# Kernel optimization log

Hardware: AMD Instinct MI355X
Metric: run time of the kernel (lower is better)

The kernel has to match this reference:

```python
import jax, jax.numpy as jnp
import numpy as np

B = 2048        # patients (segments)
K = 4           # images per patient
C = 1280        # backbone_out (tf_efficientnet_b0)
PAIRS = K * (K - 1) // 2  # torch.combinations -> 6
NCLS = 1
N_DROP = 5


def setup_inputs() -> dict:
    key = jax.random.key(0)
    ks = jax.random.split(key, 8)
    x = jax.random.normal(ks[0], (B * K, C), jnp.float32)  # detached backbone features
    ids2 = jnp.repeat(jnp.arange(B, dtype=jnp.int32), PAIRS)  # segment id per pair
    Wc = jax.random.normal(ks[1], (C, C, 2), jnp.float32) * 0.02  # Conv1d(C,C,k=2) weight
    bc = jnp.zeros((C,), jnp.float32)
    W0 = jax.random.normal(ks[2], (NCLS, C), jnp.float32) * 0.02
    b0 = jnp.zeros((NCLS,), jnp.float32)
    W1 = jax.random.normal(ks[3], (1, C), jnp.float32) * 0.02
    b1 = jnp.zeros((1,), jnp.float32)
    W2 = jax.random.normal(ks[4], (1, C), jnp.float32) * 0.02
    b2 = jnp.zeros((1,), jnp.float32)
    return dict(x=x, ids2=ids2, Wc=Wc, bc=bc, W0=W0, b0=b0, W1=W1, b1=b1, W2=W2, b2=b2)


def reference(x, ids2, Wc, bc, W0, b0, W1, b1, W2, b2):
    # --- pair combinations within each patient group of K images ---
    ii, jj = np.triu_indices(K, 1)               # static [PAIRS]
    xg = x.reshape(B, K, C)
    xa = xg[:, ii].reshape(B * PAIRS, C)         # first element of each pair
    xb = xg[:, jj].reshape(B * PAIRS, C)         # second element
    # Conv1d(C, C, kernel=2) over the length-2 pair sequence + ReLU
    xc = jax.nn.relu(xa @ Wc[:, :, 0].T + xb @ Wc[:, :, 1].T + bc)  # [P, C]

    # --- 5 fixed dropout masks (p=0.5, train-mode scaling) ---
    masks = jax.random.bernoulli(jax.random.key(42), 0.5,
                                 (N_DROP, xc.shape[0], C)).astype(xc.dtype) * 2.0
    xd = xc[None] * masks                        # [D, P, C]

    cnt = jax.ops.segment_sum(jnp.ones_like(ids2, dtype=xc.dtype),
                              ids2, num_segments=B)  # [B], == PAIRS

    def agg(W, b):
        # head -> scalar mean over classes -> segment-mean over pairs -> mean over dropouts
        z = (jnp.einsum('dpc,oc->dpo', xd, W) + b).mean(-1)          # [D, P]
        s = jax.vmap(lambda u: jax.ops.segment_sum(u, ids2, num_segments=B))(z)
        return (s / cnt).mean(0)                                      # [B]

    logits = agg(W0, b0)
    logits1 = agg(W1, b1)
    logits2 = agg(W2, b2)
    return jnp.stack([logits, logits1, logits2], axis=1)  # [B, 3]
```

## Files before the change

kernel.cpp:

```cpp
#include <hip/hip_runtime.h>


typedef __attribute__((ext_vector_type(8))) short short8;
typedef __attribute__((ext_vector_type(4))) float f32x4;

#define PLANE 15728640u
#define KS2   (0x1BD11BDAu ^ 42u)

__device__ __forceinline__ unsigned short f2bf(float f) {
  unsigned int u = __builtin_bit_cast(unsigned int, f);
  u = (u + 0x7FFFu + ((u >> 16) & 1u)) >> 16;
  return (unsigned short)u;
}
__device__ __forceinline__ float bf2f(unsigned short h) {
  unsigned int u = ((unsigned int)h) << 16;
  return __builtin_bit_cast(float, u);
}

__global__ __launch_bounds__(256) void prep(
    const float* __restrict__ x, unsigned short* __restrict__ xb,
    const float* __restrict__ Wc, unsigned short* __restrict__ Wb) {
  const int bid = blockIdx.x;
  const int t = threadIdx.x;
  if (bid < 2560) {
#pragma unroll
    for (int p = 0; p < 4; p++) {
      const int i4 = bid * 1024 + p * 256 + t;
      const float4 v = ((const float4*)x)[i4];
      ushort4 o;
      o.x = f2bf(v.x); o.y = f2bf(v.y); o.z = f2bf(v.z); o.w = f2bf(v.w);
      ((ushort4*)xb)[i4] = o;
    }
  } else {
    const int i = (bid - 2560) * 256 + t;
    const int n = i / 640;
    const int cin = (i - n * 640) * 2;
    const float4 v = *(const float4*)(Wc + n * 2560 + cin * 2);
    *(ushort2*)(Wb + n * 2560 + cin) =
        make_ushort2(f2bf(v.x), f2bf(v.z));
    *(ushort2*)(Wb + n * 2560 + 1280 + cin) =
        make_ushort2(f2bf(v.y), f2bf(v.w));
  }
}

__device__ __forceinline__ unsigned int rotl(unsigned int x, int r) {
  return __builtin_amdgcn_alignbit(x, x, 32 - r);
}

__device__ __forceinline__ unsigned int tf_msb5(const unsigned int cbase) {
  unsigned int x0[5], x1[5];
#pragma unroll
  for (int d = 0; d < 5; d++) {
    const unsigned int c = cbase + (unsigned int)d * PLANE;
    x0[d] = c;
    x1[d] = rotl(c, 13) ^ c;
  }
#define R5(r)                                                   \
  _Pragma("unroll") for (int d = 0; d < 5; d++) {               \
    x0[d] += x1[d];                                             \
    x1[d] = rotl(x1[d], (r)) ^ x0[d];                           \
  }
  R5(15) R5(26) R5(6)
#pragma unroll
  for (int d = 0; d < 5; d++) {
    const unsigned int t = x1[d] + (KS2 + 1u);
    x0[d] = x0[d] + t + 42u;
    x1[d] = rotl(t, 17) ^ x0[d];
  }
  R5(29) R5(16) R5(24)
#pragma unroll
  for (int d = 0; d < 5; d++) {
    const unsigned int t = x1[d] + 2u;
    x0[d] = x0[d] + t + KS2;
    x1[d] = rotl(t, 13) ^ x0[d];
  }
  R5(15) R5(26) R5(6)
#pragma unroll
  for (int d = 0; d < 5; d++) {
    const unsigned int t = x1[d] + 45u;
    x0[d] = x0[d] + t;
    x1[d] = rotl(t, 17) ^ x0[d];
  }
  R5(29) R5(16) R5(24)
#pragma unroll
  for (int d = 0; d < 5; d++) {
    const unsigned int t = x1[d] + (KS2 + 4u);
    x0[d] = x0[d] + t + 42u;
    x1[d] = rotl(t, 13) ^ x0[d];
  }
  R5(15) R5(26) R5(6)
#undef R5
  unsigned int z = 0;
#pragma unroll
  for (int d = 0; d < 5; d++)
    z += ((x0[d] + KS2) ^ (x1[d] + 5u)) >> 31;
  return z;
}

#define GL_LDS(g, l) __builtin_amdgcn_global_load_lds( \
    (const __attribute__((address_space(1))) unsigned int*)(g), \
    (__attribute__((address_space(3))) unsigned int*)(l), 16, 0, 0)

__global__ __launch_bounds__(256) void mixed(
    const unsigned short* __restrict__ Xb,
    const unsigned short* __restrict__ Wb,
    unsigned short* __restrict__ U0b,
    unsigned short* __restrict__ U1b)
{
  __shared__ unsigned short sA[128 * 32];
  __shared__ unsigned short sB[128 * 32];
  const int bid = blockIdx.x;
  const int t = threadIdx.x;

  const int id = bid;
  const int xcd = id & 7;
  const int slot = id >> 3;
  const int mband = xcd * 8 + slot / 20;
  const int nst = slot % 20;
  const int side = nst / 10;
  const int n0 = (nst % 10) * 128;
  const int p0 = mband * 128;

  const int lane = t & 63, w = t >> 6;
  const int wr = w >> 1, wc = w & 1;
  const int mrow = lane & 15;
  const int koff = (lane >> 4) * 8;
  const int srow = lane >> 2, schk = (lane & 3) * 8;

  unsigned short* const ldsA0 = sA + (w * 32 + 0) * 32;
  unsigned short* const ldsA1 = sA + (w * 32 + 16) * 32;
  unsigned short* const ldsB0 = sB + (w * 32 + 0) * 32;
  unsigned short* const ldsB1 = sB + (w * 32 + 16) * 32;
  const unsigned short* const gA0 = Xb + (p0 + w * 32 + srow) * 1280 + schk;
  const unsigned short* const gA1 = Xb + (p0 + w * 32 + 16 + srow) * 1280 + schk;
  const unsigned short* const gB0 =
      Wb + (n0 + w * 32 + srow) * 2560 + side * 1280 + schk;
  const unsigned short* const gB1 =
      Wb + (n0 + w * 32 + 16 + srow) * 2560 + side * 1280 + schk;

  f32x4 acc[4][4];
#pragma unroll
  for (int i = 0; i < 4; i++)
#pragma unroll
    for (int j = 0; j < 4; j++) acc[i][j] = (f32x4){0.f, 0.f, 0.f, 0.f};

  for (int k0 = 0; k0 < 1280; k0 += 32) {
    __syncthreads();
    GL_LDS(gA0 + k0, ldsA0);
    GL_LDS(gA1 + k0, ldsA1);
    GL_LDS(gB0 + k0, ldsB0);
    GL_LDS(gB1 + k0, ldsB1);
    __syncthreads();
    short8 af[4], bfr[4];
#pragma unroll
    for (int i = 0; i < 4; i++)
      af[i] = *(const short8*)(sA + (wr * 64 + i * 16 + mrow) * 32 + koff);
#pragma unroll
    for (int j = 0; j < 4; j++)
      bfr[j] = *(const short8*)(sB + (wc * 64 + j * 16 + mrow) * 32 + koff);
#pragma unroll
    for (int i = 0; i < 4; i++)
#pragma unroll
      for (int j = 0; j < 4; j++)
        acc[i][j] = __builtin_amdgcn_mfma_f32_16x16x32_bf16(af[i], bfr[j],
                                                            acc[i][j], 0, 0, 0);
  }

  unsigned short* const U = side ? U1b : U0b;
  const int mq = (lane >> 4) * 4;
  const int nn = lane & 15;
#pragma unroll
  for (int j = 0; j < 4; j++) {
    const int n = n0 + wc * 64 + j * 16 + nn;
#pragma unroll
    for (int i = 0; i < 4; i++) {
      const int prow = p0 + wr * 64 + i * 16 + mq;
#pragma unroll
      for (int rg = 0; rg < 4; rg++)
        U[(prow + rg) * 1280 + n] = f2bf(acc[i][j][rg]);
    }
  }
}

__global__ __launch_bounds__(256) void combine(
    const unsigned short* __restrict__ U0b, const unsigned short* __restrict__ U1b,
    const float* __restrict__ bc,
    const float* __restrict__ W0, const float* __restrict__ W1,
    const float* __restrict__ W2,
    const float* __restrict__ b0, const float* __restrict__ b1,
    const float* __restrict__ b2, float* __restrict__ out)
{
  const int pat = blockIdx.x;
  const int t = threadIdx.x;
  const int rbase = pat * 4 * 1280;
  float s0 = 0.f, s1 = 0.f, s2 = 0.f;

  for (int qi = 0; qi < 5; qi++) {
    const int c = qi * 256 + t;
    const float w0 = W0[c], w1 = W1[c], w2 = W2[c], bcv = bc[c];
    const float u00 = bf2f(U0b[rbase + c]);
    const float u01 = bf2f(U0b[rbase + 1280 + c]);
    const float u02 = bf2f(U0b[rbase + 2560 + c]);
    const float u11 = bf2f(U1b[rbase + 1280 + c]);
    const float u12 = bf2f(U1b[rbase + 2560 + c]);
    const float u13 = bf2f(U1b[rbase + 3840 + c]);
    const float pv[6] = {u00 + u11, u00 + u12, u00 + u13,
                         u01 + u12, u01 + u13, u02 + u13};
    const unsigned int cb = (unsigned int)(pat * 6 * 1280 + c) + 42u;
#pragma unroll
    for (int pr = 0; pr < 6; pr++) {
      float v = pv[pr] + bcv;
      v = v > 0.f ? v : 0.f;
      const unsigned int z = tf_msb5(cb + (unsigned int)(pr * 1280));
      const float tx = v * (float)(5 - (int)z);
      s0 += tx * w0; s1 += tx * w1; s2 += tx * w2;
    }
  }

#pragma unroll
  for (int off = 32; off > 0; off >>= 1) {
    s0 += __shfl_xor(s0, off); s1 += __shfl_xor(s1, off); s2 += __shfl_xor(s2, off);
  }
  __shared__ float red[4][3];
  const int lane = t & 63, w = t >> 6;
  if (lane == 0) { red[w][0] = s0; red[w][1] = s1; red[w][2] = s2; }
  __syncthreads();
  if (t == 0) {
    const float r0 = red[0][0] + red[1][0] + red[2][0] + red[3][0];
    const float r1 = red[0][1] + red[1][1] + red[2][1] + red[3][1];
    const float r2 = red[0][2] + red[1][2] + red[2][2] + red[3][2];
    out[pat * 3 + 0] = b0[0] + r0 * (1.0f / 15.0f);
    out[pat * 3 + 1] = b1[0] + r1 * (1.0f / 15.0f);
    out[pat * 3 + 2] = b2[0] + r2 * (1.0f / 15.0f);
  }
}

extern "C" void kernel_launch(void* const* d_in, const int* in_sizes, int n_in,
                              void* d_out, int out_size, void* d_ws, size_t ws_size,
                              hipStream_t stream) {
  const float* x  = (const float*)d_in[0];
  const float* Wc = (const float*)d_in[2];
  const float* bc = (const float*)d_in[3];
  const float* W0 = (const float*)d_in[4];
  const float* b0 = (const float*)d_in[5];
  const float* W1 = (const float*)d_in[6];
  const float* b1 = (const float*)d_in[7];
  const float* W2 = (const float*)d_in[8];
  const float* b2 = (const float*)d_in[9];
  float* out = (float*)d_out;

  char* ws = (char*)d_ws;
  unsigned short* xb  = (unsigned short*)ws;
  unsigned short* Wb  = (unsigned short*)(ws + 20971520);
  unsigned short* U0b = (unsigned short*)(ws + 27525120);
  unsigned short* U1b = (unsigned short*)(ws + 48496640);

  prep<<<5760, 256, 0, stream>>>(x, xb, Wc, Wb);
  mixed<<<1280, 256, 0, stream>>>(xb, Wb, U0b, U1b);
  combine<<<2048, 256, 0, stream>>>(U0b, U1b, bc, W0, W1, W2,
                                    b0, b1, b2, out);
}
```

Measured before the change: 305.6 us.

## Precompute packed dropout-mask counts in prep kernel for combine to read

Threefry mask generation moves out of the combine kernel and into the prep kernel. Prep now computes, for each element, the count of kept dropout draws and packs eight 4-bit counts per word into a workspace buffer, which combine reads back with shifts. The aim is to take the hash ALU work off combine's critical path and run it alongside the memory-bound bf16 conversion in prep. In exchange it adds roughly 8 MB of writes and reads, and puts more ALU load into prep.

```diff
diff --git a/kernel.cpp b/kernel.cpp
--- a/kernel.cpp
+++ b/kernel.cpp
@@ -17,9 +17,64 @@
   return __builtin_bit_cast(float, u);
 }
 
+__device__ __forceinline__ unsigned int rotl(unsigned int x, int r) {
+  return __builtin_amdgcn_alignbit(x, x, 32 - r);
+}
+
+__device__ __forceinline__ unsigned int tf_msb5(const unsigned int cbase) {
+  unsigned int x0[5], x1[5];
+#pragma unroll
+  for (int d = 0; d < 5; d++) {
+    const unsigned int c = cbase + (unsigned int)d * PLANE;
+    x0[d] = c;
+    x1[d] = rotl(c, 13) ^ c;
+  }
+#define R5(r)                                                   \
+  _Pragma("unroll") for (int d = 0; d < 5; d++) {               \
+    x0[d] += x1[d];                                             \
+    x1[d] = rotl(x1[d], (r)) ^ x0[d];                           \
+  }
+  R5(15) R5(26) R5(6)
+#pragma unroll
+  for (int d = 0; d < 5; d++) {
+    const unsigned int u = x1[d] + (KS2 + 1u);
+    x0[d] = x0[d] + u + 42u;
+    x1[d] = rotl(u, 17) ^ x0[d];
+  }
+  R5(29) R5(16) R5(24)
+#pragma unroll
+  for (int d = 0; d < 5; d++) {
+    const unsigned int u = x1[d] + 2u;
+    x0[d] = x0[d] + u + KS2;
+    x1[d] = rotl(u, 13) ^ x0[d];
+  }
+  R5(15) R5(26) R5(6)
+#pragma unroll
+  for (int d = 0; d < 5; d++) {
+    const unsigned int u = x1[d] + 45u;
+    x0[d] = x0[d] + u;
+    x1[d] = rotl(u, 17) ^ x0[d];
+  }
+  R5(29) R5(16) R5(24)
+#pragma unroll
+  for (int d = 0; d < 5; d++) {
+    const unsigned int u = x1[d] + (KS2 + 4u);
+    x0[d] = x0[d] + u + 42u;
+    x1[d] = rotl(u, 13) ^ x0[d];
+  }
+  R5(15) R5(26) R5(6)
+#undef R5
+  unsigned int z = 0;
+#pragma unroll
+  for (int d = 0; d < 5; d++)
+    z += ((x0[d] + KS2) ^ (x1[d] + 5u)) >> 31;
+  return z;
+}
+
 __global__ __launch_bounds__(256) void prep(
     const float* __restrict__ x, unsigned short* __restrict__ xb,
-    const float* __restrict__ Wc, unsigned short* __restrict__ Wb) {
+    const float* __restrict__ Wc, unsigned short* __restrict__ Wb,
+    unsigned int* __restrict__ Spk) {
   const int bid = blockIdx.x;
   const int t = threadIdx.x;
   if (bid < 2560) {
@@ -41,60 +96,15 @@
     *(ushort2*)(Wb + n * 2560 + 1280 + cin) =
         make_ushort2(f2bf(v.y), f2bf(v.w));
   }
-}
-
-__device__ __forceinline__ unsigned int rotl(unsigned int x, int r) {
-  return __builtin_amdgcn_alignbit(x, x, 32 - r);
-}
-
-__device__ __forceinline__ unsigned int tf_msb5(const unsigned int cbase) {
-  unsigned int x0[5], x1[5];
-#pragma unroll
-  for (int d = 0; d < 5; d++) {
-    const unsigned int c = cbase + (unsigned int)d * PLANE;
-    x0[d] = c;
-    x1[d] = rotl(c, 13) ^ c;
-  }
-#define R5(r)                                                   \
-  _Pragma("unroll") for (int d = 0; d < 5; d++) {               \
-    x0[d] += x1[d];                                             \
-    x1[d] = rotl(x1[d], (r)) ^ x0[d];                           \
-  }
-  R5(15) R5(26) R5(6)
-#pragma unroll
-  for (int d = 0; d < 5; d++) {
-    const unsigned int t = x1[d] + (KS2 + 1u);
-    x0[d] = x0[d] + t + 42u;
-    x1[d] = rotl(t, 17) ^ x0[d];
-  }
-  R5(29) R5(16) R5(24)
-#pragma unroll
-  for (int d = 0; d < 5; d++) {
-    const unsigned int t = x1[d] + 2u;
-    x0[d] = x0[d] + t + KS2;
-    x1[d] = rotl(t, 13) ^ x0[d];
-  }
-  R5(15) R5(26) R5(6)
-#pragma unroll
-  for (int d = 0; d < 5; d++) {
-    const unsigned int t = x1[d] + 45u;
-    x0[d] = x0[d] + t;
-    x1[d] = rotl(t, 17) ^ x0[d];
-  }
-  R5(29) R5(16) R5(24)
-#pragma unroll
-  for (int d = 0; d < 5; d++) {
-    const unsigned int t = x1[d] + (KS2 + 4u);
-    x0[d] = x0[d] + t + 42u;
-    x1[d] = rotl(t, 13) ^ x0[d];
-  }
-  R5(15) R5(26) R5(6)
-#undef R5
-  unsigned int z = 0;
-#pragma unroll
-  for (int d = 0; d < 5; d++)
-    z += ((x0[d] + KS2) ^ (x1[d] + 5u)) >> 31;
-  return z;
+  for (unsigned int d = (unsigned int)bid * 256u + (unsigned int)t;
+       d < 1966080u; d += 1474560u) {
+    const unsigned int bg = d * 8u + 42u;
+    unsigned int zacc = 0;
+#pragma unroll
+    for (int sub = 0; sub < 8; ++sub)
+      zacc |= tf_msb5(bg + (unsigned int)sub) << (4 * sub);
+    Spk[d] = zacc;
+  }
 }
 
 #define GL_LDS(g, l) __builtin_amdgcn_global_load_lds( \
@@ -184,7 +194,7 @@
 
 __global__ __launch_bounds__(256) void combine(
     const unsigned short* __restrict__ U0b, const unsigned short* __restrict__ U1b,
-    const float* __restrict__ bc,
+    const unsigned int* __restrict__ Spk, const float* __restrict__ bc,
     const float* __restrict__ W0, const float* __restrict__ W1,
     const float* __restrict__ W2,
     const float* __restrict__ b0, const float* __restrict__ b1,
@@ -193,6 +203,7 @@
   const int pat = blockIdx.x;
   const int t = threadIdx.x;
   const int rbase = pat * 4 * 1280;
+  const int sbase = pat * 6 * 160;
   float s0 = 0.f, s1 = 0.f, s2 = 0.f;
 
   for (int qi = 0; qi < 5; qi++) {
@@ -206,13 +217,13 @@
     const float u13 = bf2f(U1b[rbase + 3840 + c]);
     const float pv[6] = {u00 + u11, u00 + u12, u00 + u13,
                          u01 + u12, u01 + u13, u02 + u13};
-    const unsigned int cb = (unsigned int)(pat * 6 * 1280 + c) + 42u;
+    const int cd = c >> 3, cn = 4 * (c & 7);
 #pragma unroll
     for (int pr = 0; pr < 6; pr++) {
       float v = pv[pr] + bcv;
       v = v > 0.f ? v : 0.f;
-      const unsigned int z = tf_msb5(cb + (unsigned int)(pr * 1280));
-      const float tx = v * (float)(5 - (int)z);
+      const int z = (int)((Spk[sbase + pr * 160 + cd] >> cn) & 7u);
+      const float tx = v * (float)(5 - z);
       s0 += tx * w0; s1 += tx * w1; s2 += tx * w2;
     }
   }
@@ -254,9 +265,10 @@
   unsigned short* Wb  = (unsigned short*)(ws + 20971520);
   unsigned short* U0b = (unsigned short*)(ws + 27525120);
   unsigned short* U1b = (unsigned short*)(ws + 48496640);
-
-  prep<<<5760, 256, 0, stream>>>(x, xb, Wc, Wb);
+  unsigned int*   Spk = (unsigned int*)(ws + 69468160);
+
+  prep<<<5760, 256, 0, stream>>>(x, xb, Wc, Wb, Spk);
   mixed<<<1280, 256, 0, stream>>>(xb, Wb, U0b, U1b);
-  combine<<<2048, 256, 0, stream>>>(U0b, U1b, bc, W0, W1, W2,
+  combine<<<2048, 256, 0, stream>>>(U0b, U1b, Spk, bc, W0, W1, W2,
                                     b0, b1, b2, out);
 }
```

New measurement: 379.2 us. +24.1%, slower.
